# Optimization experiments

Measured on AMD Instinct MI355X. Metric: run time of the kernel, lower is better.

The kernel has to match this reference:

```python
import jax, jax.numpy as jnp
import numpy as np

B, C, H, W = 8, 128, 64, 64
C8, C2 = C // 8, C // 2


def conv1x1(x, w, b):
    # x: [B,Cin,H,W], w: [Cout,Cin], b: [Cout]
    return jnp.einsum('bchw,oc->bohw', x, w) + b[None, :, None, None]


def maxpool2(x):
    # 2x2 stride-2 max pool on [B,C,H,W]
    b, c, h, w = x.shape
    return x.reshape(b, c, h // 2, 2, w // 2, 2).max(axis=(3, 5))


def setup_inputs() -> dict:
    key = jax.random.key(0)
    ks = jax.random.split(key, 10)
    s_in = 1.0 / np.sqrt(C)
    s_c2 = 1.0 / np.sqrt(C2)
    return {
        'x': jax.random.normal(ks[0], (B, C, H, W), dtype=jnp.float32),
        'w_theta': jax.random.uniform(ks[1], (C8, C), jnp.float32, -s_in, s_in),
        'b_theta': jax.random.uniform(ks[2], (C8,), jnp.float32, -s_in, s_in),
        'w_phi': jax.random.uniform(ks[3], (C8, C), jnp.float32, -s_in, s_in),
        'b_phi': jax.random.uniform(ks[4], (C8,), jnp.float32, -s_in, s_in),
        'w_g': jax.random.uniform(ks[5], (C2, C), jnp.float32, -s_in, s_in),
        'b_g': jax.random.uniform(ks[6], (C2,), jnp.float32, -s_in, s_in),
        'w_attn': jax.random.uniform(ks[7], (C, C2), jnp.float32, -s_c2, s_c2),
        'b_attn': jax.random.uniform(ks[8], (C,), jnp.float32, -s_c2, s_c2),
        'sigma': jnp.zeros((1,), dtype=jnp.float32),
    }


def reference(x, w_theta, b_theta, w_phi, b_phi, w_g, b_g, w_attn, b_attn, sigma):
    b, ch, h, w = x.shape
    n, m = h * w, (h * w) // 4
    theta = conv1x1(x, w_theta, b_theta).reshape(b, ch // 8, n)          # [B,C8,N]
    phi = maxpool2(conv1x1(x, w_phi, b_phi)).reshape(b, ch // 8, m)      # [B,C8,M]
    attn = jax.nn.softmax(jnp.einsum('bdn,bdm->bnm', theta, phi), axis=-1)  # [B,N,M]
    g = maxpool2(conv1x1(x, w_g, b_g)).reshape(b, ch // 2, m)            # [B,C2,M]
    attn_g = jnp.einsum('bcm,bnm->bcn', g, attn).reshape(b, ch // 2, h, w)
    attn_g = conv1x1(attn_g, w_attn, b_attn)
    return x + sigma[0] * attn_g
```

## Files before the change

### kernel.cpp

```cpp
#include <hip/hip_runtime.h>
#include <hip/hip_bf16.h>
#include <math.h>
#include <string.h>

#define Bn 8
#define Cn 128
#define Nn 4096
#define Mn 1024
#define C8n 16
#define C2n 64

typedef __attribute__((ext_vector_type(8))) short short8;
typedef __attribute__((ext_vector_type(4))) float floatx4;
typedef __attribute__((ext_vector_type(4))) unsigned short ushortx4;

__device__ __forceinline__ unsigned short f2bf(float f) {
    union { float f; unsigned u; } v; v.f = f;
    unsigned r = v.u + 0x7fff + ((v.u >> 16) & 1);
    return (unsigned short)(r >> 16);
}
__device__ __forceinline__ unsigned pk2(float a, float b) {
    __hip_bfloat162 h = __float22bfloat162_rn(make_float2(a, b));
    union { __hip_bfloat162 h2; unsigned u; } cv;
    cv.h2 = h;
    return cv.u;
}

__global__ __launch_bounds__(256) void k1_pre(
    const float* __restrict__ x,
    const float* __restrict__ w_theta, const float* __restrict__ b_theta,
    const float* __restrict__ w_phi,   const float* __restrict__ b_phi,
    const float* __restrict__ w_g,     const float* __restrict__ b_g,
    unsigned short* __restrict__ thA,
    unsigned short* __restrict__ phB,
    unsigned short* __restrict__ gB)
{
    __shared__ unsigned short wA[6 * 4 * 64 * 8];
    __shared__ unsigned short xB[8 * 4 * 64 * 8];
    __shared__ unsigned short pool[80][33];
    __shared__ float biases[96];

    const int t    = threadIdx.x;
    const int b    = blockIdx.x & 7;
    const int h2   = blockIdx.x >> 3;
    const int wv   = t >> 6;
    const int lane = t & 63;
    const int q    = lane >> 4;
    const int l15  = lane & 15;
    const float L2E = 1.4426950408889634f;

    if (t < 96)
        biases[t] = (t < 16) ? b_theta[t] * L2E
                  : (t < 32) ? b_phi[t - 16] : b_g[t - 32];

    #pragma unroll
    for (int k = 0; k < 12; ++k) {
        int u  = t + k * 256;
        int oc = u >> 5, c4 = u & 31;
        const float* src = (oc < 16) ? (w_theta + oc * Cn)
                         : (oc < 32) ? (w_phi + (oc - 16) * Cn)
                                     : (w_g + (oc - 32) * Cn);
        float4 wv4 = *(const float4*)(src + c4 * 4);
        float sc = (oc < 16) ? L2E : 1.f;
        int c = c4 * 4;
        int ot = oc >> 4, kc = c >> 5, qq = (c >> 3) & 3, jj = c & 7;
        uint2 pk = { pk2(wv4.x * sc, wv4.y * sc), pk2(wv4.z * sc, wv4.w * sc) };
        *(uint2*)(wA + (((ot * 4 + kc) * 64 + qq * 16 + (oc & 15)) * 8 + jj)) = pk;
    }

    const float* xb = x + (size_t)b * Cn * Nn + h2 * 128;
    #pragma unroll
    for (int k = 0; k < 16; ++k) {
        int u   = t + k * 256;
        int pos = u & 127, c4 = u >> 7;
        int c   = c4 * 4;
        float v0 = xb[(size_t)(c + 0) * Nn + pos];
        float v1 = xb[(size_t)(c + 1) * Nn + pos];
        float v2 = xb[(size_t)(c + 2) * Nn + pos];
        float v3 = xb[(size_t)(c + 3) * Nn + pos];
        int pt = pos >> 4, kc = c >> 5, qq = (c >> 3) & 3, jj = c & 7;
        uint2 pk = { pk2(v0, v1), pk2(v2, v3) };
        *(uint2*)(xB + (((pt * 4 + kc) * 64 + qq * 16 + (pos & 15)) * 8 + jj)) = pk;
    }
    __syncthreads();

    floatx4 acc[6][2];
    #pragma unroll
    for (int ot = 0; ot < 6; ++ot)
        #pragma unroll
        for (int p2 = 0; p2 < 2; ++p2) acc[ot][p2] = (floatx4){0.f, 0.f, 0.f, 0.f};

    #pragma unroll
    for (int kc = 0; kc < 4; ++kc) {
        short8 Bf0 = *(const short8*)(xB + ((wv * 4 + kc) * 64 + lane) * 8);
        short8 Bf1 = *(const short8*)(xB + (((wv + 4) * 4 + kc) * 64 + lane) * 8);
        #pragma unroll
        for (int ot = 0; ot < 6; ++ot) {
            short8 Af = *(const short8*)(wA + ((ot * 4 + kc) * 64 + lane) * 8);
            acc[ot][0] = __builtin_amdgcn_mfma_f32_16x16x32_bf16(Af, Bf0, acc[ot][0], 0, 0, 0);
            acc[ot][1] = __builtin_amdgcn_mfma_f32_16x16x32_bf16(Af, Bf1, acc[ot][1], 0, 0, 0);
        }
    }

    #pragma unroll
    for (int p2 = 0; p2 < 2; ++p2) {
        const int pt = wv + p2 * 4;
        float v0 = acc[0][p2][0] + biases[q * 4 + 0];
        float v1 = acc[0][p2][1] + biases[q * 4 + 1];
        float v2 = acc[0][p2][2] + biases[q * 4 + 2];
        float v3 = acc[0][p2][3] + biases[q * 4 + 3];
        uint2 pk = { pk2(v0, v1), pk2(v2, v3) };
        *(uint2*)(thA + ((((size_t)b * 256 + h2 * 8 + pt) * 2 + (q >> 1)) * 128
                         + l15 * 8 + (q & 1) * 4)) = pk;
    }

    #pragma unroll
    for (int ot = 1; ot < 6; ++ot) {
        #pragma unroll
        for (int r = 0; r < 4; ++r) {
            float vmax = fmaxf(acc[ot][0][r], acc[ot][1][r]);
            float pmax = fmaxf(vmax, __shfl_xor(vmax, 1, 64));
            if ((l15 & 1) == 0) {
                int oc = (ot - 1) * 16 + q * 4 + r;
                int w2 = wv * 8 + (l15 >> 1);
                pool[oc][w2] = f2bf(pmax + biases[16 + oc]);
            }
        }
    }
    __syncthreads();

    if (t < 64) {
        int w2h = t >> 5, ml = (t >> 1) & 15, dh = t & 1;
        int w2 = w2h * 16 + ml;
        ushortx4 lo, hi;
        #pragma unroll
        for (int j = 0; j < 4; ++j) { lo[j] = pool[dh * 8 + j][w2];
                                      hi[j] = pool[dh * 8 + 4 + j][w2]; }
        unsigned short* dst = phB + (((size_t)b * 64 + h2 * 2 + w2h) * 2 + dh) * 128 + ml * 8;
        *(ushortx4*)dst = lo;
        *(ushortx4*)(dst + 4) = hi;
    }
    {
        int c = t >> 2, sq = t & 3;
        ushortx4 lo, hi;
        #pragma unroll
        for (int j = 0; j < 8; ++j) {
            int w2 = (j & 1) * 16 + sq * 4 + (j >> 1);
            unsigned short v = pool[16 + c][w2];
            if (j < 4) lo[j] = v; else hi[j - 4] = v;
        }
        unsigned short* dst = gB + ((((size_t)b * 32 + h2) * 4 + (c >> 4)) * 4 + sq) * 128
                              + (c & 15) * 8;
        *(ushortx4*)dst = lo;
        *(ushortx4*)(dst + 4) = hi;
    }
}

__global__ __launch_bounds__(256, 4) void k2_attn(
    const float* __restrict__ x,
    const unsigned short* __restrict__ thA,
    const unsigned short* __restrict__ phB,
    const unsigned short* __restrict__ gB,
    const float* __restrict__ w_attn, const float* __restrict__ b_attn,
    const float* __restrict__ sigma_p,
    float* __restrict__ out)
{
    __shared__ __attribute__((aligned(16))) char smem[22016];
    char*  Pall  = smem + 16384;
    float* battn = (float*)(smem + 21504);

    const int tid  = threadIdx.x;
    const int wave = tid >> 6;
    const int lane = tid & 63;
    const int q    = lane >> 4;
    const int l15  = lane & 15;
    const int b    = blockIdx.x & 7;
    const int nb   = blockIdx.x >> 3;
    const int t    = wave & 1;
    const int h    = wave >> 1;
    const int ntile = nb * 2 + t;
    const int nw   = ntile * 16;
    char* Pbase = Pall + wave * 1280;

    const float sg = sigma_p[0];

    short8 thf = {};
    if (q < 2)
        thf = *(const short8*)(thA + ((((size_t)b * 256 + ntile) * 2 + q) * 16 + l15) * 8);

    floatx4 O[4];
    #pragma unroll
    for (int cs = 0; cs < 4; ++cs) O[cs] = (floatx4){0.f, 0.f, 0.f, 0.f};
    float L[4] = {0.f, 0.f, 0.f, 0.f};

    const unsigned short* phh = phB + (size_t)b * 16384 + h * 32 * 256;
    const unsigned short* ghh = gB  + (size_t)b * 65536 + h * 16 * 2048;

    #pragma unroll 2
    for (int s = 0; s < 16; ++s) {
        const unsigned short* pt0 = phh + s * 512;
        short8 bf0 = {}, bf1 = {};
        if (q < 2) {
            bf0 = *(const short8*)(pt0 + (q * 16 + l15) * 8);
            bf1 = *(const short8*)(pt0 + 256 + (q * 16 + l15) * 8);
        }
        const unsigned short* gc = ghh + s * 2048;
        short8 Bf0 = *(const short8*)(gc + ((0 * 4 + q) * 16 + l15) * 8);
        short8 Bf1 = *(const short8*)(gc + ((1 * 4 + q) * 16 + l15) * 8);
        short8 Bf2 = *(const short8*)(gc + ((2 * 4 + q) * 16 + l15) * 8);
        short8 Bf3 = *(const short8*)(gc + ((3 * 4 + q) * 16 + l15) * 8);

        floatx4 S0 = __builtin_amdgcn_mfma_f32_16x16x32_bf16(
                         thf, bf0, (floatx4){0.f, 0.f, 0.f, 0.f}, 0, 0, 0);
        floatx4 S1 = __builtin_amdgcn_mfma_f32_16x16x32_bf16(
                         thf, bf1, (floatx4){0.f, 0.f, 0.f, 0.f}, 0, 0, 0);
        #pragma unroll
        for (int r = 0; r < 4; ++r) {
            float pa = exp2f(S0[r]);
            float pb = exp2f(S1[r]);
            L[r] += pa + pb;
            *(unsigned*)(Pbase + (q * 4 + r) * 80 + l15 * 4) = pk2(pa, pb);
        }

        short8 Af = *(const short8*)(Pbase + l15 * 80 + q * 16);
        O[0] = __builtin_amdgcn_mfma_f32_16x16x32_bf16(Af, Bf0, O[0], 0, 0, 0);
        O[1] = __builtin_amdgcn_mfma_f32_16x16x32_bf16(Af, Bf1, O[1], 0, 0, 0);
        O[2] = __builtin_amdgcn_mfma_f32_16x16x32_bf16(Af, Bf2, O[2], 0, 0, 0);
        O[3] = __builtin_amdgcn_mfma_f32_16x16x32_bf16(Af, Bf3, O[3], 0, 0, 0);
    }

    #pragma unroll
    for (int d = 1; d <= 8; d <<= 1)
        #pragma unroll
        for (int r = 0; r < 4; ++r) L[r] += __shfl_xor(L[r], d, 64);

    __syncthreads();
    float* Lpart = (float*)(smem + 8704);
    if (h == 1) {
        #pragma unroll
        for (int r = 0; r < 4; ++r) {
            float* Orow = (float*)(smem + t * 4352 + (q * 4 + r) * 272);
            #pragma unroll
            for (int cs = 0; cs < 4; ++cs) Orow[cs * 16 + l15] = O[cs][r];
            if (l15 == 0) Lpart[t * 16 + q * 4 + r] = L[r];
        }
    }
    if (tid < 128) battn[tid] = b_attn[tid];
    __syncthreads();
    unsigned short* Obuf = (unsigned short*)(smem + 16384);
    if (h == 0) {
        #pragma unroll
        for (int r = 0; r < 4; ++r) {
            const float* Orow = (const float*)(smem + t * 4352 + (q * 4 + r) * 272);
            #pragma unroll
            for (int cs = 0; cs < 4; ++cs) O[cs][r] += Orow[cs * 16 + l15];
            L[r] += Lpart[t * 16 + q * 4 + r];
        }
        float inv[4];
        #pragma unroll
        for (int r = 0; r < 4; ++r) inv[r] = 1.0f / L[r];
        unsigned short* Ob = Obuf + t * 1152;
        #pragma unroll
        for (int cs = 0; cs < 4; ++cs)
            #pragma unroll
            for (int r = 0; r < 4; ++r)
                Ob[(q * 4 + r) * 72 + cs * 16 + l15] = f2bf(O[cs][r] * inv[r]);
    }
    __syncthreads();

    {
        unsigned short* wAe = (unsigned short*)smem;
        #pragma unroll
        for (int k = 0; k < 8; ++k) {
            int i = tid + k * 256;
            float4 wv = ((const float4*)w_attn)[i];
            int o = i >> 4, c = (i & 15) * 4;
            uint2 pk = { pk2(wv.x, wv.y), pk2(wv.z, wv.w) };
            *(uint2*)(wAe + ((o >> 4) * 2 + (c >> 5)) * 512 + (o & 15) * 32 + (c & 31)) = pk;
        }
    }
    __syncthreads();

    {
        const unsigned short* wAe = (const unsigned short*)smem;
        const unsigned short* Ob  = Obuf + t * 1152;
        short8 B0 = *(const short8*)(Ob + l15 * 72 + q * 8);
        short8 B1 = *(const short8*)(Ob + l15 * 72 + 32 + q * 8);
        const float* xw = x   + (size_t)b * Cn * Nn + nw + l15;
        float*       ow = out + (size_t)b * Cn * Nn + nw + l15;
        #pragma unroll
        for (int ot4 = 0; ot4 < 4; ++ot4) {
            const int ot = h * 4 + ot4;
            short8 A0 = *(const short8*)(wAe + (ot * 2 + 0) * 512 + l15 * 32 + q * 8);
            short8 A1 = *(const short8*)(wAe + (ot * 2 + 1) * 512 + l15 * 32 + q * 8);
            floatx4 D = __builtin_amdgcn_mfma_f32_16x16x32_bf16(
                            A0, B0, (floatx4){0.f, 0.f, 0.f, 0.f}, 0, 0, 0);
            D = __builtin_amdgcn_mfma_f32_16x16x32_bf16(A1, B1, D, 0, 0, 0);
            #pragma unroll
            for (int r = 0; r < 4; ++r) {
                int o = ot * 16 + q * 4 + r;
                float v = D[r] + battn[o];
                ow[(size_t)o * Nn] = xw[(size_t)o * Nn] + sg * v;
            }
        }
    }
}

extern "C" void kernel_launch(void* const* d_in, const int* in_sizes, int n_in,
                              void* d_out, int out_size, void* d_ws, size_t ws_size,
                              hipStream_t stream) {
    const float* x       = (const float*)d_in[0];
    const float* w_theta = (const float*)d_in[1];
    const float* b_theta = (const float*)d_in[2];
    const float* w_phi   = (const float*)d_in[3];
    const float* b_phi   = (const float*)d_in[4];
    const float* w_g     = (const float*)d_in[5];
    const float* b_g     = (const float*)d_in[6];
    const float* w_attn  = (const float*)d_in[7];
    const float* b_attn  = (const float*)d_in[8];
    const float* sigma   = (const float*)d_in[9];
    float* out = (float*)d_out;

    unsigned short* thA = (unsigned short*)d_ws;
    unsigned short* phB = thA + 524288;
    unsigned short* gBp = phB + 131072;

    k1_pre<<<256, 256, 0, stream>>>(x, w_theta, b_theta, w_phi, b_phi,
                                    w_g, b_g, thA, phB, gBp);
    k2_attn<<<1024, 256, 0, stream>>>(x, thA, phB, gBp, w_attn, b_attn, sigma, out);
}
```

Baseline: 110.3 us.

## Split attention KV range across four waves per block; widen pre-kernel to 512 threads

In the attention kernel, each wave now handles both query tiles of the block over a quarter of the key range, instead of two waves splitting the keys in half per tile. This reuses each loaded phi/g fragment across two query tiles and halves the per-wave loop length. Partial outputs and row sums from all four waves are reduced through a larger shared buffer, which costs extra LDS, more accumulator registers and a wider reduction. The pre-kernel doubles its threads so each wave computes half the output-channel tiles, giving more waves to hide latency.

Result: no change. 109.8 us (-0.5%).

```diff
diff --git a/kernel.cpp b/kernel.cpp
--- a/kernel.cpp
+++ b/kernel.cpp
@@ -26,7 +26,7 @@
     return cv.u;
 }
 
-__global__ __launch_bounds__(256) void k1_pre(
+__global__ __launch_bounds__(512) void k1_pre(
     const float* __restrict__ x,
     const float* __restrict__ w_theta, const float* __restrict__ b_theta,
     const float* __restrict__ w_phi,   const float* __restrict__ b_phi,
@@ -43,10 +43,12 @@
     const int t    = threadIdx.x;
     const int b    = blockIdx.x & 7;
     const int h2   = blockIdx.x >> 3;
-    const int wv   = t >> 6;
+    const int w    = t >> 6;
     const int lane = t & 63;
     const int q    = lane >> 4;
     const int l15  = lane & 15;
+    const int p    = w & 3;
+    const int oh   = w >> 2;
     const float L2E = 1.4426950408889634f;
 
     if (t < 96)
@@ -54,8 +56,8 @@
                   : (t < 32) ? b_phi[t - 16] : b_g[t - 32];
 
     #pragma unroll
-    for (int k = 0; k < 12; ++k) {
-        int u  = t + k * 256;
+    for (int k = 0; k < 6; ++k) {
+        int u  = t + k * 512;
         int oc = u >> 5, c4 = u & 31;
         const float* src = (oc < 16) ? (w_theta + oc * Cn)
                          : (oc < 32) ? (w_phi + (oc - 16) * Cn)
@@ -70,8 +72,8 @@
 
     const float* xb = x + (size_t)b * Cn * Nn + h2 * 128;
     #pragma unroll
-    for (int k = 0; k < 16; ++k) {
-        int u   = t + k * 256;
+    for (int k = 0; k < 8; ++k) {
+        int u   = t + k * 512;
         int pos = u & 127, c4 = u >> 7;
         int c   = c4 * 4;
         float v0 = xb[(size_t)(c + 0) * Nn + pos];
@@ -84,45 +86,49 @@
     }
     __syncthreads();
 
-    floatx4 acc[6][2];
-    #pragma unroll
-    for (int ot = 0; ot < 6; ++ot)
-        #pragma unroll
-        for (int p2 = 0; p2 < 2; ++p2) acc[ot][p2] = (floatx4){0.f, 0.f, 0.f, 0.f};
+    floatx4 acc[3][2];
+    #pragma unroll
+    for (int o3 = 0; o3 < 3; ++o3)
+        #pragma unroll
+        for (int p2 = 0; p2 < 2; ++p2) acc[o3][p2] = (floatx4){0.f, 0.f, 0.f, 0.f};
 
     #pragma unroll
     for (int kc = 0; kc < 4; ++kc) {
-        short8 Bf0 = *(const short8*)(xB + ((wv * 4 + kc) * 64 + lane) * 8);
-        short8 Bf1 = *(const short8*)(xB + (((wv + 4) * 4 + kc) * 64 + lane) * 8);
-        #pragma unroll
-        for (int ot = 0; ot < 6; ++ot) {
-            short8 Af = *(const short8*)(wA + ((ot * 4 + kc) * 64 + lane) * 8);
-            acc[ot][0] = __builtin_amdgcn_mfma_f32_16x16x32_bf16(Af, Bf0, acc[ot][0], 0, 0, 0);
-            acc[ot][1] = __builtin_amdgcn_mfma_f32_16x16x32_bf16(Af, Bf1, acc[ot][1], 0, 0, 0);
-        }
-    }
-
-    #pragma unroll
-    for (int p2 = 0; p2 < 2; ++p2) {
-        const int pt = wv + p2 * 4;
-        float v0 = acc[0][p2][0] + biases[q * 4 + 0];
-        float v1 = acc[0][p2][1] + biases[q * 4 + 1];
-        float v2 = acc[0][p2][2] + biases[q * 4 + 2];
-        float v3 = acc[0][p2][3] + biases[q * 4 + 3];
-        uint2 pk = { pk2(v0, v1), pk2(v2, v3) };
-        *(uint2*)(thA + ((((size_t)b * 256 + h2 * 8 + pt) * 2 + (q >> 1)) * 128
-                         + l15 * 8 + (q & 1) * 4)) = pk;
-    }
-
-    #pragma unroll
-    for (int ot = 1; ot < 6; ++ot) {
+        short8 Bf0 = *(const short8*)(xB + ((p * 4 + kc) * 64 + lane) * 8);
+        short8 Bf1 = *(const short8*)(xB + (((p + 4) * 4 + kc) * 64 + lane) * 8);
+        #pragma unroll
+        for (int o3 = 0; o3 < 3; ++o3) {
+            short8 Af = *(const short8*)(wA + (((oh * 3 + o3) * 4 + kc) * 64 + lane) * 8);
+            acc[o3][0] = __builtin_amdgcn_mfma_f32_16x16x32_bf16(Af, Bf0, acc[o3][0], 0, 0, 0);
+            acc[o3][1] = __builtin_amdgcn_mfma_f32_16x16x32_bf16(Af, Bf1, acc[o3][1], 0, 0, 0);
+        }
+    }
+
+    if (oh == 0) {
+        #pragma unroll
+        for (int p2 = 0; p2 < 2; ++p2) {
+            const int pt = p + p2 * 4;
+            float v0 = acc[0][p2][0] + biases[q * 4 + 0];
+            float v1 = acc[0][p2][1] + biases[q * 4 + 1];
+            float v2 = acc[0][p2][2] + biases[q * 4 + 2];
+            float v3 = acc[0][p2][3] + biases[q * 4 + 3];
+            uint2 pk = { pk2(v0, v1), pk2(v2, v3) };
+            *(uint2*)(thA + ((((size_t)b * 256 + h2 * 8 + pt) * 2 + (q >> 1)) * 128
+                             + l15 * 8 + (q & 1) * 4)) = pk;
+        }
+    }
+
+    #pragma unroll
+    for (int o3 = 0; o3 < 3; ++o3) {
+        const int ot = oh * 3 + o3;
+        if (ot == 0) continue;
         #pragma unroll
         for (int r = 0; r < 4; ++r) {
-            float vmax = fmaxf(acc[ot][0][r], acc[ot][1][r]);
+            float vmax = fmaxf(acc[o3][0][r], acc[o3][1][r]);
             float pmax = fmaxf(vmax, __shfl_xor(vmax, 1, 64));
             if ((l15 & 1) == 0) {
                 int oc = (ot - 1) * 16 + q * 4 + r;
-                int w2 = wv * 8 + (l15 >> 1);
+                int w2 = p * 8 + (l15 >> 1);
                 pool[oc][w2] = f2bf(pmax + biases[16 + oc]);
             }
         }
@@ -140,7 +146,7 @@
         *(ushortx4*)dst = lo;
         *(ushortx4*)(dst + 4) = hi;
     }
-    {
+    if (t < 256) {
         int c = t >> 2, sq = t & 3;
         ushortx4 lo, hi;
         #pragma unroll
@@ -165,9 +171,10 @@
     const float* __restrict__ sigma_p,
     float* __restrict__ out)
 {
-    __shared__ __attribute__((aligned(16))) char smem[22016];
-    char*  Pall  = smem + 16384;
-    float* battn = (float*)(smem + 21504);
+    __shared__ __attribute__((aligned(16))) char smem[38400];
+    float* Lpart = (float*)(smem + 32768);
+    unsigned short* Obuf = (unsigned short*)(smem + 33280);
+    float* battn = (float*)(smem + 37888);
 
     const int tid  = threadIdx.x;
     const int wave = tid >> 6;
@@ -175,29 +182,31 @@
     const int q    = lane >> 4;
     const int l15  = lane & 15;
     const int b    = blockIdx.x & 7;
-    const int nb   = blockIdx.x >> 3;
-    const int t    = wave & 1;
-    const int h    = wave >> 1;
-    const int ntile = nb * 2 + t;
-    const int nw   = ntile * 16;
-    char* Pbase = Pall + wave * 1280;
+    const int ng   = blockIdx.x >> 3;
+    char* Pbase = smem + wave * 2560;
 
     const float sg = sigma_p[0];
 
-    short8 thf = {};
-    if (q < 2)
-        thf = *(const short8*)(thA + ((((size_t)b * 256 + ntile) * 2 + q) * 16 + l15) * 8);
-
-    floatx4 O[4];
-    #pragma unroll
-    for (int cs = 0; cs < 4; ++cs) O[cs] = (floatx4){0.f, 0.f, 0.f, 0.f};
-    float L[4] = {0.f, 0.f, 0.f, 0.f};
-
-    const unsigned short* phh = phB + (size_t)b * 16384 + h * 32 * 256;
-    const unsigned short* ghh = gB  + (size_t)b * 65536 + h * 16 * 2048;
+    short8 thf[2] = {{}, {}};
+    if (q < 2) {
+        #pragma unroll
+        for (int t = 0; t < 2; ++t)
+            thf[t] = *(const short8*)(thA +
+                ((((size_t)b * 256 + (ng * 2 + t)) * 2 + q) * 16 + l15) * 8);
+    }
+
+    floatx4 O[2][4];
+    #pragma unroll
+    for (int t = 0; t < 2; ++t)
+        #pragma unroll
+        for (int cs = 0; cs < 4; ++cs) O[t][cs] = (floatx4){0.f, 0.f, 0.f, 0.f};
+    float L[2][4] = {{0.f,0.f,0.f,0.f},{0.f,0.f,0.f,0.f}};
+
+    const unsigned short* phh = phB + (size_t)b * 16384 + wave * 4096;
+    const unsigned short* ghh = gB  + (size_t)b * 65536 + wave * 16384;
 
     #pragma unroll 2
-    for (int s = 0; s < 16; ++s) {
+    for (int s = 0; s < 8; ++s) {
         const unsigned short* pt0 = phh + s * 512;
         short8 bf0 = {}, bf1 = {};
         if (q < 2) {
@@ -210,61 +219,64 @@
         short8 Bf2 = *(const short8*)(gc + ((2 * 4 + q) * 16 + l15) * 8);
         short8 Bf3 = *(const short8*)(gc + ((3 * 4 + q) * 16 + l15) * 8);
 
-        floatx4 S0 = __builtin_amdgcn_mfma_f32_16x16x32_bf16(
-                         thf, bf0, (floatx4){0.f, 0.f, 0.f, 0.f}, 0, 0, 0);
-        floatx4 S1 = __builtin_amdgcn_mfma_f32_16x16x32_bf16(
-                         thf, bf1, (floatx4){0.f, 0.f, 0.f, 0.f}, 0, 0, 0);
-        #pragma unroll
-        for (int r = 0; r < 4; ++r) {
-            float pa = exp2f(S0[r]);
-            float pb = exp2f(S1[r]);
-            L[r] += pa + pb;
-            *(unsigned*)(Pbase + (q * 4 + r) * 80 + l15 * 4) = pk2(pa, pb);
-        }
-
-        short8 Af = *(const short8*)(Pbase + l15 * 80 + q * 16);
-        O[0] = __builtin_amdgcn_mfma_f32_16x16x32_bf16(Af, Bf0, O[0], 0, 0, 0);
-        O[1] = __builtin_amdgcn_mfma_f32_16x16x32_bf16(Af, Bf1, O[1], 0, 0, 0);
-        O[2] = __builtin_amdgcn_mfma_f32_16x16x32_bf16(Af, Bf2, O[2], 0, 0, 0);
-        O[3] = __builtin_amdgcn_mfma_f32_16x16x32_bf16(Af, Bf3, O[3], 0, 0, 0);
+        #pragma unroll
+        for (int t = 0; t < 2; ++t) {
+            floatx4 S0 = __builtin_amdgcn_mfma_f32_16x16x32_bf16(
+                             thf[t], bf0, (floatx4){0.f, 0.f, 0.f, 0.f}, 0, 0, 0);
+            floatx4 S1 = __builtin_amdgcn_mfma_f32_16x16x32_bf16(
+                             thf[t], bf1, (floatx4){0.f, 0.f, 0.f, 0.f}, 0, 0, 0);
+            #pragma unroll
+            for (int r = 0; r < 4; ++r) {
+                float pa = exp2f(S0[r]);
+                float pb = exp2f(S1[r]);
+                L[t][r] += pa + pb;
+                *(unsigned*)(Pbase + t * 1280 + (q * 4 + r) * 80 + l15 * 4) = pk2(pa, pb);
+            }
+        }
+
+        #pragma unroll
+        for (int t = 0; t < 2; ++t) {
+            short8 Af = *(const short8*)(Pbase + t * 1280 + l15 * 80 + q * 16);
+            O[t][0] = __builtin_amdgcn_mfma_f32_16x16x32_bf16(Af, Bf0, O[t][0], 0, 0, 0);
+            O[t][1] = __builtin_amdgcn_mfma_f32_16x16x32_bf16(Af, Bf1, O[t][1], 0, 0, 0);
+            O[t][2] = __builtin_amdgcn_mfma_f32_16x16x32_bf16(Af, Bf2, O[t][2], 0, 0, 0);
+            O[t][3] = __builtin_amdgcn_mfma_f32_16x16x32_bf16(Af, Bf3, O[t][3], 0, 0, 0);
+        }
     }
 
     #pragma unroll
     for (int d = 1; d <= 8; d <<= 1)
         #pragma unroll
-        for (int r = 0; r < 4; ++r) L[r] += __shfl_xor(L[r], d, 64);
-
-    __syncthreads();
-    float* Lpart = (float*)(smem + 8704);
-    if (h == 1) {
-        #pragma unroll
-        for (int r = 0; r < 4; ++r) {
-            float* Orow = (float*)(smem + t * 4352 + (q * 4 + r) * 272);
-            #pragma unroll
-            for (int cs = 0; cs < 4; ++cs) Orow[cs * 16 + l15] = O[cs][r];
-            if (l15 == 0) Lpart[t * 16 + q * 4 + r] = L[r];
-        }
+        for (int t = 0; t < 2; ++t)
+            #pragma unroll
+            for (int r = 0; r < 4; ++r) L[t][r] += __shfl_xor(L[t][r], d, 64);
+
+    __syncthreads();
+    {
+        #pragma unroll
+        for (int t = 0; t < 2; ++t)
+            #pragma unroll
+            for (int r = 0; r < 4; ++r) {
+                float* row = (float*)(smem + wave * 8192 + (t * 16 + q * 4 + r) * 256);
+                #pragma unroll
+                for (int cs = 0; cs < 4; ++cs) row[cs * 16 + l15] = O[t][cs][r];
+                if (l15 == 0) Lpart[wave * 32 + t * 16 + q * 4 + r] = L[t][r];
+            }
     }
     if (tid < 128) battn[tid] = b_attn[tid];
     __syncthreads();
-    unsigned short* Obuf = (unsigned short*)(smem + 16384);
-    if (h == 0) {
-        #pragma unroll
-        for (int r = 0; r < 4; ++r) {
-            const float* Orow = (const float*)(smem + t * 4352 + (q * 4 + r) * 272);
-            #pragma unroll
-            for (int cs = 0; cs < 4; ++cs) O[cs][r] += Orow[cs * 16 + l15];
-            L[r] += Lpart[t * 16 + q * 4 + r];
-        }
-        float inv[4];
-        #pragma unroll
-        for (int r = 0; r < 4; ++r) inv[r] = 1.0f / L[r];
-        unsigned short* Ob = Obuf + t * 1152;
-        #pragma unroll
-        for (int cs = 0; cs < 4; ++cs)
-            #pragma unroll
-            for (int r = 0; r < 4; ++r)
-                Ob[(q * 4 + r) * 72 + cs * 16 + l15] = f2bf(O[cs][r] * inv[r]);
+    {
+        #pragma unroll
+        for (int k = 0; k < 8; ++k) {
+            const int rho = wave * 8 + k;
+            float acc = 0.f, Ls = 0.f;
+            #pragma unroll
+            for (int w2 = 0; w2 < 4; ++w2) {
+                acc += *(const float*)(smem + w2 * 8192 + rho * 256 + lane * 4);
+                Ls  += Lpart[w2 * 32 + rho];
+            }
+            Obuf[(rho >> 4) * 1152 + (rho & 15) * 72 + lane] = f2bf(acc / Ls);
+        }
     }
     __syncthreads();
 
@@ -282,6 +294,9 @@
     __syncthreads();
 
     {
+        const int t  = wave & 1;
+        const int ohh = wave >> 1;
+        const int nw = (ng * 2 + t) * 16;
         const unsigned short* wAe = (const unsigned short*)smem;
         const unsigned short* Ob  = Obuf + t * 1152;
         short8 B0 = *(const short8*)(Ob + l15 * 72 + q * 8);
@@ -290,7 +305,7 @@
         float*       ow = out + (size_t)b * Cn * Nn + nw + l15;
         #pragma unroll
         for (int ot4 = 0; ot4 < 4; ++ot4) {
-            const int ot = h * 4 + ot4;
+            const int ot = ohh * 4 + ot4;
             short8 A0 = *(const short8*)(wAe + (ot * 2 + 0) * 512 + l15 * 32 + q * 8);
             short8 A1 = *(const short8*)(wAe + (ot * 2 + 1) * 512 + l15 * 32 + q * 8);
             floatx4 D = __builtin_amdgcn_mfma_f32_16x16x32_bf16(
@@ -325,7 +340,7 @@
     unsigned short* phB = thA + 524288;
     unsigned short* gBp = phB + 131072;
 
-    k1_pre<<<256, 256, 0, stream>>>(x, w_theta, b_theta, w_phi, b_phi,
+    k1_pre<<<256, 512, 0, stream>>>(x, w_theta, b_theta, w_phi, b_phi,
                                     w_g, b_g, thA, phB, gBp);
     k2_attn<<<1024, 256, 0, stream>>>(x, thA, phB, gBp, w_attn, b_attn, sigma, out);
 }
```
